# Optimization experiments

Hardware: AMD Instinct MI355X
Metric: run time of the kernel (lower is better)

## Reference

```python
import jax, jax.numpy as jnp
import numpy as np

N, E, G, T, H, ED, IN_D, OUT_D = 50000, 1600000, 64, 5, 64, 9, 10, 3
EPS = 1e-6

def _seg_mean(vals, seg, num):
    s = jax.ops.segment_sum(vals, seg, num_segments=num)
    c = jax.ops.segment_sum(jnp.ones((vals.shape[0],), vals.dtype), seg, num_segments=num)
    return s / jnp.maximum(c, 1.0)[:, None], c

def per_graph_edge_norm(edge_attr, edge_graph, num_graphs):
    # standardize each edge-feature column per graph (zero-shot transfer trick)
    mu, _ = _seg_mean(edge_attr, edge_graph, num_graphs)
    sq, _ = _seg_mean(edge_attr * edge_attr, edge_graph, num_graphs)
    var = jnp.maximum(sq - mu * mu, 0.0)
    std = jnp.sqrt(var)
    return (edge_attr - mu[edge_graph]) / (std[edge_graph] + EPS)

def setup_inputs() -> dict:
    key = jax.random.key(0)
    ks = jax.random.split(key, 24)
    s = 0.05  # weight scale to keep ReLU chains stable
    inp = {
        'x': jax.random.normal(ks[0], (N, IN_D), jnp.float32),
        'edge_index': jax.random.randint(ks[1], (2, E), 0, N),
        'edge_attr': jax.random.normal(ks[2], (E, ED), jnp.float32),
        'batch': jnp.sort(jax.random.randint(ks[3], (N,), 0, G)),
        'lift_W1': jax.random.normal(ks[4], (IN_D, H), jnp.float32) * s,
        'lift_b1': jnp.zeros((H,), jnp.float32),
        'lift_W2': jax.random.normal(ks[5], (H, H), jnp.float32) * s,
        'lift_b2': jnp.zeros((H,), jnp.float32),
        'Wself': jax.random.normal(ks[6], (T, H, H), jnp.float32) * s,
        'bself': jnp.zeros((T, H), jnp.float32),
        'msg_W0': jax.random.normal(ks[7], (T, H + ED, H), jnp.float32) * s,
        'msg_b0': jnp.zeros((T, H), jnp.float32),
        'msg_W1': jax.random.normal(ks[8], (T, H, H), jnp.float32) * s,
        'msg_b1': jnp.zeros((T, H), jnp.float32),
        'msg_W2': jax.random.normal(ks[9], (T, H, H), jnp.float32) * s,
        'msg_b2': jnp.zeros((T, H), jnp.float32),
        'gate_W': jax.random.normal(ks[10], (T, 1, H), jnp.float32) * s,
        'gate_b': jnp.zeros((T, H), jnp.float32),
        'proj_W1': jax.random.normal(ks[11], (H, H), jnp.float32) * s,
        'proj_b1': jnp.zeros((H,), jnp.float32),
        'proj_W2': jax.random.normal(ks[12], (H, OUT_D), jnp.float32) * s,
        'proj_b2': jnp.zeros((OUT_D,), jnp.float32),
    }
    return inp

def _gno(x, edge_index, edge_attr, batch,
         lift_W1, lift_b1, lift_W2, lift_b2,
         Wself, bself, msg_W0, msg_b0, msg_W1, msg_b1, msg_W2, msg_b2,
         gate_W, gate_b, proj_W1, proj_b1, proj_W2, proj_b2):
    src, dst = edge_index[0], edge_index[1]
    edge_graph = batch[src]
    ea = per_graph_edge_norm(edge_attr, edge_graph, G)  # cols 0:9 == all cols
    log_diag_y = x[:, 4:5]                               # [N,1]
    v0 = jax.nn.relu(x @ lift_W1 + lift_b1) @ lift_W2 + lift_b2  # lift
    v = v0
    for t in range(T):
        # gather -> per-edge MLP -> scatter-mean (AdmittanceKernelLayer)
        h = jnp.concatenate([v[src], ea], axis=-1)              # [E, H+ED]
        h = jax.nn.relu(h @ msg_W0[t] + msg_b0[t])
        h = jax.nn.relu(h @ msg_W1[t] + msg_b1[t])
        m = h @ msg_W2[t] + msg_b2[t]                           # [E, H]
        agg, _ = _seg_mean(m, dst, N)                           # mean aggregation
        gate = jax.nn.sigmoid(log_diag_y @ gate_W[t] + gate_b[t])  # [N,H]
        v = jax.nn.relu(v @ Wself[t] + bself[t] + agg + v0) * gate
        # dropout inactive at inference
    out = jax.nn.relu(v @ proj_W1 + proj_b1) @ proj_W2 + proj_b2  # project
    return out

def reference(x, edge_index, edge_attr, batch,
              lift_W1, lift_b1, lift_W2, lift_b2,
              Wself, bself, msg_W0, msg_b0, msg_W1, msg_b1, msg_W2, msg_b2,
              gate_W, gate_b, proj_W1, proj_b1, proj_W2, proj_b2):
    return _gno(x, edge_index, edge_attr, batch,
                lift_W1, lift_b1, lift_W2, lift_b2,
                Wself, bself, msg_W0, msg_b0, msg_W1, msg_b1, msg_W2, msg_b2,
                gate_W, gate_b, proj_W1, proj_b1, proj_W2, proj_b2)
```

## Files before the change

### kernel.cpp

```cpp
#include <hip/hip_runtime.h>
#include <math.h>

#define NN 50000
#define NE 1600000
#define NG 64
#define NT 5
#define NH 64
#define NED 9
#define NIN 10
#define NOUT 3
#define EPSF 1e-6f
#define NSUB (NE / 16)

typedef __attribute__((ext_vector_type(8))) short s8v;
typedef __attribute__((ext_vector_type(4))) short s4v;
typedef __attribute__((ext_vector_type(4))) float f32x4;

__device__ __forceinline__ unsigned short f2bf(float f) {
    union { float f; unsigned int u; } v; v.f = f;
    unsigned int r = v.u + 0x7FFFu + ((v.u >> 16) & 1u);
    return (unsigned short)(r >> 16);
}
__device__ __forceinline__ float bf2f(unsigned short b) {
    union { unsigned int u; float f; } v; v.u = ((unsigned int)b) << 16;
    return v.f;
}

__global__ void stats_kernel(const int* __restrict__ ei, const float* __restrict__ ea,
                             const int* __restrict__ batch,
                             float* __restrict__ ssum, float* __restrict__ ssq,
                             float* __restrict__ scnt, int* __restrict__ ecnt) {
    __shared__ float lsum[NG * NED];
    __shared__ float lsq[NG * NED];
    __shared__ float lcnt[NG];
    for (int i = threadIdx.x; i < NG * NED; i += blockDim.x) { lsum[i] = 0.f; lsq[i] = 0.f; }
    for (int i = threadIdx.x; i < NG; i += blockDim.x) lcnt[i] = 0.f;
    __syncthreads();
    int lane = threadIdx.x & 63;
    int stride = gridDim.x * blockDim.x;
    for (int e = blockIdx.x * blockDim.x + threadIdx.x; e < NE; e += stride) {
        int s = ei[e];
        int g = batch[s];
        atomicAdd(&ecnt[ei[NE + e]], 1);
        float a[NED];
#pragma unroll
        for (int d = 0; d < NED; ++d) a[d] = ea[(size_t)e * NED + d];
        int g0 = __builtin_amdgcn_readfirstlane(g);
        if (__all(g == g0)) {
            float sv[NED], qv[NED];
#pragma unroll
            for (int d = 0; d < NED; ++d) { sv[d] = a[d]; qv[d] = a[d] * a[d]; }
#pragma unroll
            for (int off = 32; off; off >>= 1) {
#pragma unroll
                for (int d = 0; d < NED; ++d) {
                    sv[d] += __shfl_down(sv[d], off);
                    qv[d] += __shfl_down(qv[d], off);
                }
            }
            if (lane == 0) {
#pragma unroll
                for (int d = 0; d < NED; ++d) {
                    atomicAdd(&lsum[g0 * NED + d], sv[d]);
                    atomicAdd(&lsq[g0 * NED + d], qv[d]);
                }
                atomicAdd(&lcnt[g0], 64.f);
            }
        } else {
            atomicAdd(&lcnt[g], 1.0f);
#pragma unroll
            for (int d = 0; d < NED; ++d) {
                atomicAdd(&lsum[g * NED + d], a[d]);
                atomicAdd(&lsq[g * NED + d], a[d] * a[d]);
            }
        }
    }
    __syncthreads();
    for (int i = threadIdx.x; i < NG * NED; i += blockDim.x) {
        atomicAdd(&ssum[i], lsum[i]);
        atomicAdd(&ssq[i], lsq[i]);
    }
    for (int i = threadIdx.x; i < NG; i += blockDim.x) atomicAdd(&scnt[i], lcnt[i]);
}

__global__ void stats_fin(const float* __restrict__ ssum, const float* __restrict__ ssq,
                          const float* __restrict__ scnt,
                          float* __restrict__ mu, float* __restrict__ rstd) {
    int i = blockIdx.x * blockDim.x + threadIdx.x;
    if (i >= NG * NED) return;
    int g = i / NED;
    float c = fmaxf(scnt[g], 1.0f);
    float m = ssum[i] / c;
    float q = ssq[i] / c;
    float var = fmaxf(q - m * m, 0.f);
    mu[i] = m;
    rstd[i] = 1.0f / (sqrtf(var) + EPSF);
}

__global__ void scan1_kernel(const int* __restrict__ ecnt, int* __restrict__ partial) {
    __shared__ int sm[256];
    int i = blockIdx.x * 256 + threadIdx.x;
    sm[threadIdx.x] = (i < NN) ? ecnt[i] : 0;
    __syncthreads();
    for (int off = 128; off; off >>= 1) {
        if (threadIdx.x < off) sm[threadIdx.x] += sm[threadIdx.x + off];
        __syncthreads();
    }
    if (threadIdx.x == 0) partial[blockIdx.x] = sm[0];
}
__global__ void scan2_kernel(int* __restrict__ partial, int nb) {
    __shared__ int sm[256];
    int t = threadIdx.x;
    sm[t] = (t < nb) ? partial[t] : 0;
    __syncthreads();
    for (int off = 1; off < 256; off <<= 1) {
        int v = (t >= off) ? sm[t - off] : 0;
        __syncthreads();
        sm[t] += v;
        __syncthreads();
    }
    if (t < nb) partial[t] = (t ? sm[t - 1] : 0);
}
__global__ void scan3_kernel(const int* __restrict__ ecnt, const int* __restrict__ partial,
                             int* __restrict__ offs) {
    __shared__ int sm[256];
    int b = blockIdx.x, t = threadIdx.x, i = b * 256 + t;
    int x = (i < NN) ? ecnt[i] : 0;
    sm[t] = x;
    __syncthreads();
    for (int off = 1; off < 256; off <<= 1) {
        int v = (t >= off) ? sm[t - off] : 0;
        __syncthreads();
        sm[t] += v;
        __syncthreads();
    }
    if (i < NN) offs[i] = sm[t] - x + partial[b];
}

__global__ void permute_kernel(const int* __restrict__ ei, const int* __restrict__ offs,
                               int* __restrict__ cursor, int* __restrict__ perm) {
    int stride = gridDim.x * blockDim.x;
    for (int e = blockIdx.x * blockDim.x + threadIdx.x; e < NE; e += stride) {
        int d = ei[NE + e];
        int pos = offs[d] + atomicAdd(&cursor[d], 1);
        perm[pos] = e;
    }
}

__global__ void pack_kernel(const int* __restrict__ perm, const int* __restrict__ ei,
                            const float* __restrict__ ea, const int* __restrict__ batch,
                            const float* __restrict__ mu, const float* __restrict__ rstd,
                            int* __restrict__ srcPerm, int* __restrict__ dstPerm,
                            unsigned short* __restrict__ eaN) {
    int stride = gridDim.x * blockDim.x;
    for (int p = blockIdx.x * blockDim.x + threadIdx.x; p < NE; p += stride) {
        int e = perm[p];
        int s = ei[e], d = ei[NE + e];
        int g = batch[s];
        srcPerm[p] = s;
        dstPerm[p] = d;
#pragma unroll
        for (int k = 0; k < NED; ++k) {
            float val = (ea[(size_t)e * NED + k] - mu[g * NED + k]) * rstd[g * NED + k];
            eaN[(size_t)k * NE + p] = f2bf(val);
        }
    }
}

__global__ __launch_bounds__(256) void lift_kernel(
    const float* __restrict__ x,
    const float* __restrict__ W1, const float* __restrict__ b1,
    const float* __restrict__ W2, const float* __restrict__ b2,
    float* __restrict__ v0, float* __restrict__ v, float* __restrict__ ldy) {
    __shared__ float sW1[NIN * NH];
    __shared__ __align__(16) float sW2[NH][NH];
    __shared__ float sb1[NH], sb2[NH];
    for (int i = threadIdx.x; i < NIN * NH; i += blockDim.x) sW1[i] = W1[i];
    for (int i = threadIdx.x; i < NH * NH; i += blockDim.x) {
        int k = i >> 6, j = i & 63;
        sW2[j][k] = W2[i];
    }
    for (int i = threadIdx.x; i < NH; i += blockDim.x) { sb1[i] = b1[i]; sb2[i] = b2[i]; }
    __syncthreads();
    int stride = gridDim.x * blockDim.x;
    for (int n = blockIdx.x * blockDim.x + threadIdx.x; n < NN; n += stride) {
        float xr[NIN];
#pragma unroll
        for (int k = 0; k < NIN; ++k) xr[k] = x[(size_t)n * NIN + k];
        ldy[n] = xr[4];
        float h[NH];
#pragma unroll
        for (int j = 0; j < NH; ++j) {
            float acc = sb1[j];
#pragma unroll
            for (int k = 0; k < NIN; ++k) acc += xr[k] * sW1[k * NH + j];
            h[j] = fmaxf(acc, 0.f);
        }
#pragma unroll
        for (int j = 0; j < NH; ++j) {
            float acc = sb2[j];
#pragma unroll
            for (int k = 0; k < NH; k += 4) {
                float4 w = *(const float4*)&sW2[j][k];
                acc += h[k] * w.x + h[k + 1] * w.y + h[k + 2] * w.z + h[k + 3] * w.w;
            }
            v0[(size_t)n * NH + j] = acc;
            v[(size_t)n * NH + j] = acc;
        }
    }
}

__device__ __forceinline__ void gemm_acc68(const float* __restrict__ Ab,
                                           const float* __restrict__ Wb,
                                           int K, int te, int tj, float acc[4][4]) {
#pragma unroll 4
    for (int k = 0; k < K; ++k) {
        float4 a = *(const float4*)(Ab + k * 68 + (te << 2));
        float4 b = *(const float4*)(Wb + (k << 6) + (tj << 2));
        acc[0][0] = fmaf(a.x, b.x, acc[0][0]);
        acc[0][1] = fmaf(a.x, b.y, acc[0][1]);
        acc[0][2] = fmaf(a.x, b.z, acc[0][2]);
        acc[0][3] = fmaf(a.x, b.w, acc[0][3]);
        acc[1][0] = fmaf(a.y, b.x, acc[1][0]);
        acc[1][1] = fmaf(a.y, b.y, acc[1][1]);
        acc[1][2] = fmaf(a.y, b.z, acc[1][2]);
        acc[1][3] = fmaf(a.y, b.w, acc[1][3]);
        acc[2][0] = fmaf(a.z, b.x, acc[2][0]);
        acc[2][1] = fmaf(a.z, b.y, acc[2][1]);
        acc[2][2] = fmaf(a.z, b.z, acc[2][2]);
        acc[2][3] = fmaf(a.z, b.w, acc[2][3]);
        acc[3][0] = fmaf(a.w, b.x, acc[3][0]);
        acc[3][1] = fmaf(a.w, b.y, acc[3][1]);
        acc[3][2] = fmaf(a.w, b.z, acc[3][2]);
        acc[3][3] = fmaf(a.w, b.w, acc[3][3]);
    }
}

__global__ __launch_bounds__(256, 4) void u_kernel(
    const float* __restrict__ v, const float* __restrict__ W0v,
    const float* __restrict__ b0, float* __restrict__ U) {
    __shared__ __align__(16) float Vt[64][68];
    __shared__ __align__(16) float sW[64][64];
    __shared__ float sb[64];
    const int tid = threadIdx.x;
    const int base = blockIdx.x * 64;
    const int te = tid >> 4, tj = tid & 15;

    {
        int r = tid >> 2;
        int kb = (tid & 3) << 4;
        int n = base + r;
        const float4* vrow = (const float4*)(v + (size_t)n * NH + kb);
#pragma unroll
        for (int q = 0; q < 4; ++q) {
            float4 f = (n < NN) ? vrow[q] : make_float4(0.f, 0.f, 0.f, 0.f);
            int k = kb + q * 4;
            Vt[k + 0][r] = f.x; Vt[k + 1][r] = f.y; Vt[k + 2][r] = f.z; Vt[k + 3][r] = f.w;
        }
    }
    for (int i4 = tid; i4 < 64 * 16; i4 += 256) {
        int k = i4 >> 4, c4 = i4 & 15;
        *(float4*)&sW[k][c4 * 4] = *(const float4*)(W0v + (size_t)k * 64 + c4 * 4);
    }
    if (tid < 64) sb[tid] = b0[tid];
    __syncthreads();

    float acc[4][4];
    {
        float b0_ = sb[tj * 4 + 0], b1_ = sb[tj * 4 + 1], b2_ = sb[tj * 4 + 2], b3_ = sb[tj * 4 + 3];
#pragma unroll
        for (int ee = 0; ee < 4; ++ee) { acc[ee][0] = b0_; acc[ee][1] = b1_; acc[ee][2] = b2_; acc[ee][3] = b3_; }
    }
    gemm_acc68(&Vt[0][0], &sW[0][0], 64, te, tj, acc);

#pragma unroll
    for (int ee = 0; ee < 4; ++ee) {
        int n = base + te * 4 + ee;
        if (n < NN)
            *(float4*)&U[(size_t)n * NH + tj * 4] =
                make_float4(acc[ee][0], acc[ee][1], acc[ee][2], acc[ee][3]);
    }
}

__global__ __launch_bounds__(256, 4) void edge4_kernel(
    const int* __restrict__ srcPerm, const int* __restrict__ dstPerm,
    const unsigned short* __restrict__ eaN,
    const float* __restrict__ W0e, const float* __restrict__ W1, const float* __restrict__ b1,
    const float* __restrict__ U, float* __restrict__ nodesum) {
    __shared__ __align__(16) float sWe[NED][64];
    __shared__ __align__(16) short W1frag[8][64][8];
    __shared__ __align__(16) short h0bf[4][16 * 64];
    __shared__ __align__(16) float h1s[4][16 * 64];
    __shared__ int sDstS[4][16];

    const int tid = threadIdx.x;
    const int lane = tid & 63, w = tid >> 6;
    const int l15 = lane & 15, l4 = lane >> 4;

    for (int i4 = tid; i4 < NED * 16; i4 += 256) {
        int k = i4 >> 4, c4 = i4 & 15;
        *(float4*)&sWe[k][c4 * 4] = *(const float4*)(W0e + (size_t)k * 64 + c4 * 4);
    }
    for (int idx = tid; idx < 2 * 4 * 64; idx += 256) {
        int kc = idx >> 8, c = (idx >> 6) & 3, ln = idx & 63;
        int fl15 = ln & 15, fl4 = ln >> 4;
        int col = 16 * c + fl15;
        s8v frag;
#pragma unroll
        for (int j = 0; j < 8; ++j) {
            int k = kc * 32 + fl4 * 8 + j;
            frag[j] = (short)f2bf(W1[(size_t)k * 64 + col]);
        }
        *(s8v*)&W1frag[kc * 4 + c][ln][0] = frag;
    }
    float b1r[4];
#pragma unroll
    for (int c = 0; c < 4; ++c) b1r[c] = b1[16 * c + l15];
    __syncthreads();

    short* myh0 = h0bf[w];
    float* myh1 = h1s[w];
    int*   myd  = sDstS[w];
    const int gw = blockIdx.x * 4 + w;
    const int nw = gridDim.x * 4;

    for (int st = gw; st < NSUB; st += nw) {
        const int e16 = st * 16;
        if (lane < 16) myd[lane] = dstPerm[e16 + lane];

        int4 s4 = *(const int4*)(srcPerm + e16 + 4 * l4);
        ushort4 eu[NED];
#pragma unroll
        for (int d = 0; d < NED; ++d)
            eu[d] = *(const ushort4*)(eaN + (size_t)d * NE + e16 + 4 * l4);

        float acc0[4][4];
        {
            const int* sp = (const int*)&s4;
#pragma unroll
            for (int ee = 0; ee < 4; ++ee) {
                float4 u4 = *(const float4*)(U + (size_t)sp[ee] * NH + 4 * l15);
                acc0[ee][0] = u4.x; acc0[ee][1] = u4.y; acc0[ee][2] = u4.z; acc0[ee][3] = u4.w;
            }
        }
#pragma unroll
        for (int d = 0; d < NED; ++d) {
            float4 wv = *(const float4*)&sWe[d][4 * l15];
            float a0 = bf2f(eu[d].x), a1 = bf2f(eu[d].y), a2 = bf2f(eu[d].z), a3 = bf2f(eu[d].w);
            acc0[0][0] = fmaf(a0, wv.x, acc0[0][0]); acc0[0][1] = fmaf(a0, wv.y, acc0[0][1]);
            acc0[0][2] = fmaf(a0, wv.z, acc0[0][2]); acc0[0][3] = fmaf(a0, wv.w, acc0[0][3]);
            acc0[1][0] = fmaf(a1, wv.x, acc0[1][0]); acc0[1][1] = fmaf(a1, wv.y, acc0[1][1]);
            acc0[1][2] = fmaf(a1, wv.z, acc0[1][2]); acc0[1][3] = fmaf(a1, wv.w, acc0[1][3]);
            acc0[2][0] = fmaf(a2, wv.x, acc0[2][0]); acc0[2][1] = fmaf(a2, wv.y, acc0[2][1]);
            acc0[2][2] = fmaf(a2, wv.z, acc0[2][2]); acc0[2][3] = fmaf(a2, wv.w, acc0[2][3]);
            acc0[3][0] = fmaf(a3, wv.x, acc0[3][0]); acc0[3][1] = fmaf(a3, wv.y, acc0[3][1]);
            acc0[3][2] = fmaf(a3, wv.z, acc0[3][2]); acc0[3][3] = fmaf(a3, wv.w, acc0[3][3]);
        }

#pragma unroll
        for (int ee = 0; ee < 4; ++ee) {
            int row = 4 * l4 + ee;
            s4v p;
            p[0] = (short)f2bf(fmaxf(acc0[ee][0], 0.f));
            p[1] = (short)f2bf(fmaxf(acc0[ee][1], 0.f));
            p[2] = (short)f2bf(fmaxf(acc0[ee][2], 0.f));
            p[3] = (short)f2bf(fmaxf(acc0[ee][3], 0.f));
            *(s4v*)((char*)myh0 + row * 128 + ((l15 * 8) ^ ((row & 7) << 4))) = p;
        }

        f32x4 acc[4];
#pragma unroll
        for (int c = 0; c < 4; ++c) {
            float b = b1r[c];
            acc[c][0] = b; acc[c][1] = b; acc[c][2] = b; acc[c][3] = b;
        }
        {
            const char* abase = (const char*)myh0 + l15 * 128;
            const int aswz = (l15 & 7) << 4;
#pragma unroll
            for (int kc = 0; kc < 2; ++kc) {
                s8v af = *(const s8v*)(abase + ((l4 * 16 + kc * 64) ^ aswz));
#pragma unroll
                for (int c = 0; c < 4; ++c) {
                    s8v bf = *(const s8v*)&W1frag[kc * 4 + c][lane][0];
                    acc[c] = __builtin_amdgcn_mfma_f32_16x16x32_bf16(af, bf, acc[c], 0, 0, 0);
                }
            }
        }

        int dFirst = myd[0];
        int dLast = myd[15];
        if (dFirst == dLast) {
#pragma unroll
            for (int c = 0; c < 4; ++c) {
                float vs = fmaxf(acc[c][0], 0.f) + fmaxf(acc[c][1], 0.f) +
                           fmaxf(acc[c][2], 0.f) + fmaxf(acc[c][3], 0.f);
                vs += __shfl_xor(vs, 16);
                vs += __shfl_xor(vs, 32);
                if (l4 == 0)
                    atomicAdd(&nodesum[(size_t)dFirst * NH + 16 * c + l15], vs);
            }
        } else {
#pragma unroll
            for (int r = 0; r < 4; ++r) {
                int row = 4 * l4 + r;
#pragma unroll
                for (int c = 0; c < 4; ++c)
                    myh1[row * 64 + ((16 * c + l15) ^ (l4 * 8))] = fmaxf(acc[c][r], 0.f);
            }
            int cur = dFirst;
            float a = myh1[lane];
#pragma unroll
            for (int i = 1; i < 16; ++i) {
                int dn = myd[i];
                float hv = myh1[i * 64 + (lane ^ ((i >> 2) * 8))];
                if (dn != cur) {
                    atomicAdd(&nodesum[(size_t)cur * NH + lane], a);
                    cur = dn;
                    a = hv;
                } else {
                    a += hv;
                }
            }
            atomicAdd(&nodesum[(size_t)cur * NH + lane], a);
        }
    }
}

__global__ __launch_bounds__(256, 2) void update3_kernel(
    const float* __restrict__ Wself, const float* __restrict__ bself,
    const float* __restrict__ W2, const float* __restrict__ b2,
    const float* __restrict__ gWt, const float* __restrict__ gbt,
    const float* __restrict__ v0, const float* __restrict__ ldy,
    const int* __restrict__ ecnt, const float* __restrict__ nodesum,
    float* __restrict__ v) {
    __shared__ __align__(16) float Vt[64][68];
    __shared__ __align__(16) float St[64][68];
    __shared__ __align__(16) float sWs[64][64];
    __shared__ __align__(16) float sW2[64][64];
    __shared__ float sbs[64], sb2[64], sgw[64], sgb[64];
    const int tid = threadIdx.x;
    const int base = blockIdx.x * 64;
    const int te = tid >> 4, tj = tid & 15;

    {
        int r = tid >> 2;
        int kb = (tid & 3) << 4;
        int n = base + r;
        const float4* vrow = (const float4*)(v + (size_t)n * NH + kb);
        const float4* srow = (const float4*)(nodesum + (size_t)n * NH + kb);
#pragma unroll
        for (int q = 0; q < 4; ++q) {
            float4 f = (n < NN) ? vrow[q] : make_float4(0.f, 0.f, 0.f, 0.f);
            float4 g = (n < NN) ? srow[q] : make_float4(0.f, 0.f, 0.f, 0.f);
            int k = kb + q * 4;
            Vt[k + 0][r] = f.x; Vt[k + 1][r] = f.y; Vt[k + 2][r] = f.z; Vt[k + 3][r] = f.w;
            St[k + 0][r] = g.x; St[k + 1][r] = g.y; St[k + 2][r] = g.z; St[k + 3][r] = g.w;
        }
    }
    for (int i4 = tid; i4 < 64 * 16; i4 += 256) {
        int k = i4 >> 4, c4 = i4 & 15;
        *(float4*)&sWs[k][c4 * 4] = *(const float4*)(Wself + (size_t)k * 64 + c4 * 4);
        *(float4*)&sW2[k][c4 * 4] = *(const float4*)(W2 + (size_t)k * 64 + c4 * 4);
    }
    if (tid < 64) { sbs[tid] = bself[tid]; sb2[tid] = b2[tid]; sgw[tid] = gWt[tid]; sgb[tid] = gbt[tid]; }
    __syncthreads();

    float acc1[4][4], acc2[4][4];
    {
        float b0_ = sbs[tj * 4 + 0], b1_ = sbs[tj * 4 + 1], b2_ = sbs[tj * 4 + 2], b3_ = sbs[tj * 4 + 3];
#pragma unroll
        for (int ee = 0; ee < 4; ++ee) {
            acc1[ee][0] = b0_; acc1[ee][1] = b1_; acc1[ee][2] = b2_; acc1[ee][3] = b3_;
            acc2[ee][0] = 0.f; acc2[ee][1] = 0.f; acc2[ee][2] = 0.f; acc2[ee][3] = 0.f;
        }
    }
    gemm_acc68(&Vt[0][0], &sWs[0][0], 64, te, tj, acc1);
    gemm_acc68(&St[0][0], &sW2[0][0], 64, te, tj, acc2);

    float gw0 = sgw[tj * 4 + 0], gw1 = sgw[tj * 4 + 1], gw2 = sgw[tj * 4 + 2], gw3 = sgw[tj * 4 + 3];
    float gb0 = sgb[tj * 4 + 0], gb1 = sgb[tj * 4 + 1], gb2 = sgb[tj * 4 + 2], gb3 = sgb[tj * 4 + 3];
    float bb0 = sb2[tj * 4 + 0], bb1 = sb2[tj * 4 + 1], bb2 = sb2[tj * 4 + 2], bb3 = sb2[tj * 4 + 3];
#pragma unroll
    for (int ee = 0; ee < 4; ++ee) {
        int n = base + te * 4 + ee;
        if (n >= NN) continue;
        float cnt = (float)ecnt[n];
        float has = (cnt > 0.5f) ? 1.f : 0.f;
        float dninv = has / fmaxf(cnt, 1.f);
        float ld = ldy[n];
        float4 v0r = *(const float4*)&v0[(size_t)n * NH + tj * 4];
        float z0 = acc1[ee][0] + acc2[ee][0] * dninv + bb0 * has + v0r.x;
        float z1 = acc1[ee][1] + acc2[ee][1] * dninv + bb1 * has + v0r.y;
        float z2 = acc1[ee][2] + acc2[ee][2] * dninv + bb2 * has + v0r.z;
        float z3 = acc1[ee][3] + acc2[ee][3] * dninv + bb3 * has + v0r.w;
        float g0 = 1.f / (1.f + expf(-(ld * gw0 + gb0)));
        float g1 = 1.f / (1.f + expf(-(ld * gw1 + gb1)));
        float g2 = 1.f / (1.f + expf(-(ld * gw2 + gb2)));
        float g3 = 1.f / (1.f + expf(-(ld * gw3 + gb3)));
        *(float4*)&v[(size_t)n * NH + tj * 4] =
            make_float4(fmaxf(z0, 0.f) * g0, fmaxf(z1, 0.f) * g1,
                        fmaxf(z2, 0.f) * g2, fmaxf(z3, 0.f) * g3);
    }
}

__global__ __launch_bounds__(256) void proj_kernel(
    const float* __restrict__ v,
    const float* __restrict__ pW1, const float* __restrict__ pb1,
    const float* __restrict__ pW2, const float* __restrict__ pb2,
    float* __restrict__ out) {
    __shared__ __align__(16) float sW1[NH][NH];
    __shared__ float sb1[NH];
    __shared__ float sW2[NH * NOUT];
    __shared__ float sb2[NOUT];
    for (int i = threadIdx.x; i < NH * NH; i += blockDim.x) {
        int k = i >> 6, j = i & 63;
        sW1[j][k] = pW1[i];
    }
    for (int i = threadIdx.x; i < NH; i += blockDim.x) sb1[i] = pb1[i];
    for (int i = threadIdx.x; i < NH * NOUT; i += blockDim.x) sW2[i] = pW2[i];
    for (int i = threadIdx.x; i < NOUT; i += blockDim.x) sb2[i] = pb2[i];
    __syncthreads();
    int stride = gridDim.x * blockDim.x;
    for (int n = blockIdx.x * blockDim.x + threadIdx.x; n < NN; n += stride) {
        float vr[NH];
        const float4* vp = (const float4*)(v + (size_t)n * NH);
#pragma unroll
        for (int q = 0; q < NH / 4; ++q) {
            float4 f = vp[q];
            vr[4 * q + 0] = f.x; vr[4 * q + 1] = f.y; vr[4 * q + 2] = f.z; vr[4 * q + 3] = f.w;
        }
        float o0 = sb2[0], o1 = sb2[1], o2 = sb2[2];
#pragma unroll
        for (int j = 0; j < NH; ++j) {
            float acc = sb1[j];
#pragma unroll
            for (int k = 0; k < NH; k += 4) {
                float4 w = *(const float4*)&sW1[j][k];
                acc += vr[k] * w.x + vr[k + 1] * w.y + vr[k + 2] * w.z + vr[k + 3] * w.w;
            }
            float h = fmaxf(acc, 0.f);
            o0 += h * sW2[j * NOUT + 0];
            o1 += h * sW2[j * NOUT + 1];
            o2 += h * sW2[j * NOUT + 2];
        }
        out[(size_t)n * NOUT + 0] = o0;
        out[(size_t)n * NOUT + 1] = o1;
        out[(size_t)n * NOUT + 2] = o2;
    }
}

extern "C" void kernel_launch(void* const* d_in, const int* in_sizes, int n_in,
                              void* d_out, int out_size, void* d_ws, size_t ws_size,
                              hipStream_t stream) {
    (void)in_sizes; (void)n_in; (void)out_size; (void)ws_size;
    const float* x     = (const float*)d_in[0];
    const int*   ei    = (const int*)d_in[1];
    const float* ea    = (const float*)d_in[2];
    const int*   batch = (const int*)d_in[3];
    const float* lW1   = (const float*)d_in[4];
    const float* lb1   = (const float*)d_in[5];
    const float* lW2   = (const float*)d_in[6];
    const float* lb2   = (const float*)d_in[7];
    const float* Wself = (const float*)d_in[8];
    const float* bself = (const float*)d_in[9];
    const float* mW0   = (const float*)d_in[10];
    const float* mb0   = (const float*)d_in[11];
    const float* mW1   = (const float*)d_in[12];
    const float* mb1   = (const float*)d_in[13];
    const float* mW2   = (const float*)d_in[14];
    const float* mb2   = (const float*)d_in[15];
    const float* gW    = (const float*)d_in[16];
    const float* gb    = (const float*)d_in[17];
    const float* pW1   = (const float*)d_in[18];
    const float* pb1   = (const float*)d_in[19];
    const float* pW2   = (const float*)d_in[20];
    const float* pb2   = (const float*)d_in[21];
    float* out = (float*)d_out;
    float* ws  = (float*)d_ws;

    float* nodesum = ws;
    float* v0   = nodesum + (size_t)NN * NH;
    float* v    = v0 + (size_t)NN * NH;
    float* U    = v + (size_t)NN * NH;
    float* ldy  = U + (size_t)NN * NH;
    float* mu   = ldy + NN;
    float* rstd = mu + NG * NED;
    float* ssum = rstd + NG * NED;
    float* ssq  = ssum + NG * NED;
    float* scnt = ssq + NG * NED;
    int*   ecnt   = (int*)(scnt + NG);
    int*   cursor = ecnt + NN;
    int*   offs    = cursor + NN;
    int*   partial = offs + NN;
    int*   srcPerm = partial + 256;
    int*   dstPerm = srcPerm + NE;
    unsigned short* eaN = (unsigned short*)(dstPerm + NE);
    int*   perm = (int*)nodesum;

    const int NBLK = (NN + 63) / 64;
    const int SBLK = (NN + 255) / 256;

    hipMemsetAsync(ssum, 0, ((size_t)(2 * NG * NED + NG) + 2 * NN) * sizeof(float), stream);

    stats_kernel<<<512, 256, 0, stream>>>(ei, ea, batch, ssum, ssq, scnt, ecnt);
    stats_fin<<<3, 256, 0, stream>>>(ssum, ssq, scnt, mu, rstd);
    scan1_kernel<<<SBLK, 256, 0, stream>>>(ecnt, partial);
    scan2_kernel<<<1, 256, 0, stream>>>(partial, SBLK);
    scan3_kernel<<<SBLK, 256, 0, stream>>>(ecnt, partial, offs);
    permute_kernel<<<2048, 256, 0, stream>>>(ei, offs, cursor, perm);
    pack_kernel<<<2048, 256, 0, stream>>>(perm, ei, ea, batch, mu, rstd, srcPerm, dstPerm, eaN);
    lift_kernel<<<200, 256, 0, stream>>>(x, lW1, lb1, lW2, lb2, v0, v, ldy);

    for (int t = 0; t < NT; ++t) {
        const float* W0t = mW0 + (size_t)t * (NH + NED) * NH;
        hipMemsetAsync(nodesum, 0, (size_t)NN * NH * sizeof(float), stream);
        u_kernel<<<NBLK, 256, 0, stream>>>(v, W0t, mb0 + (size_t)t * NH, U);
        edge4_kernel<<<1024, 256, 0, stream>>>(
            srcPerm, dstPerm, eaN,
            W0t + (size_t)NH * NH,
            mW1 + (size_t)t * NH * NH, mb1 + (size_t)t * NH,
            U, nodesum);
        update3_kernel<<<NBLK, 256, 0, stream>>>(
            Wself + (size_t)t * NH * NH, bself + (size_t)t * NH,
            mW2 + (size_t)t * NH * NH, mb2 + (size_t)t * NH,
            gW + (size_t)t * NH, gb + (size_t)t * NH,
            v0, ldy, ecnt, nodesum, v);
    }
    proj_kernel<<<200, 256, 0, stream>>>(v, pW1, pb1, pW2, pb2, out);
}
```

Baseline: 1.366 ms.

## Store U in bf16, prefetch next edge tile, and deterministic per-block stats reduction

The per-node U projection is now written as bf16, halving the bytes the edge kernel gathers per source node. The edge kernel software-prefetches the next tile's source indices, destinations and edge features into registers, and keeps destinations in a register read via shuffles instead of LDS. The stats kernel drops the wave-uniform shuffle reduction, writes per-block partials without global atomics, and adds a merge kernel that sums them. Trade-offs are bf16 rounding of U, extra register pressure from prefetching, and a serial merge loop over 1024 blocks.

```diff
diff --git a/kernel.cpp b/kernel.cpp
--- a/kernel.cpp
+++ b/kernel.cpp
@@ -11,6 +11,8 @@
 #define NOUT 3
 #define EPSF 1e-6f
 #define NSUB (NE / 16)
+#define STATS_BLKS 1024
+#define STATS_SLICE (2 * NG * NED + NG)
 
 typedef __attribute__((ext_vector_type(8))) short s8v;
 typedef __attribute__((ext_vector_type(4))) short s4v;
@@ -26,61 +28,48 @@
     return v.f;
 }
 
-__global__ void stats_kernel(const int* __restrict__ ei, const float* __restrict__ ea,
-                             const int* __restrict__ batch,
-                             float* __restrict__ ssum, float* __restrict__ ssq,
-                             float* __restrict__ scnt, int* __restrict__ ecnt) {
+__global__ __launch_bounds__(256) void stats_kernel(
+    const int* __restrict__ ei, const float* __restrict__ ea,
+    const int* __restrict__ batch,
+    float* __restrict__ blockAcc, int* __restrict__ ecnt) {
     __shared__ float lsum[NG * NED];
     __shared__ float lsq[NG * NED];
     __shared__ float lcnt[NG];
     for (int i = threadIdx.x; i < NG * NED; i += blockDim.x) { lsum[i] = 0.f; lsq[i] = 0.f; }
     for (int i = threadIdx.x; i < NG; i += blockDim.x) lcnt[i] = 0.f;
     __syncthreads();
-    int lane = threadIdx.x & 63;
     int stride = gridDim.x * blockDim.x;
     for (int e = blockIdx.x * blockDim.x + threadIdx.x; e < NE; e += stride) {
         int s = ei[e];
         int g = batch[s];
         atomicAdd(&ecnt[ei[NE + e]], 1);
-        float a[NED];
-#pragma unroll
-        for (int d = 0; d < NED; ++d) a[d] = ea[(size_t)e * NED + d];
-        int g0 = __builtin_amdgcn_readfirstlane(g);
-        if (__all(g == g0)) {
-            float sv[NED], qv[NED];
-#pragma unroll
-            for (int d = 0; d < NED; ++d) { sv[d] = a[d]; qv[d] = a[d] * a[d]; }
-#pragma unroll
-            for (int off = 32; off; off >>= 1) {
-#pragma unroll
-                for (int d = 0; d < NED; ++d) {
-                    sv[d] += __shfl_down(sv[d], off);
-                    qv[d] += __shfl_down(qv[d], off);
-                }
-            }
-            if (lane == 0) {
-#pragma unroll
-                for (int d = 0; d < NED; ++d) {
-                    atomicAdd(&lsum[g0 * NED + d], sv[d]);
-                    atomicAdd(&lsq[g0 * NED + d], qv[d]);
-                }
-                atomicAdd(&lcnt[g0], 64.f);
-            }
-        } else {
-            atomicAdd(&lcnt[g], 1.0f);
-#pragma unroll
-            for (int d = 0; d < NED; ++d) {
-                atomicAdd(&lsum[g * NED + d], a[d]);
-                atomicAdd(&lsq[g * NED + d], a[d] * a[d]);
-            }
-        }
-    }
-    __syncthreads();
+        atomicAdd(&lcnt[g], 1.0f);
+#pragma unroll
+        for (int d = 0; d < NED; ++d) {
+            float a = ea[(size_t)e * NED + d];
+            atomicAdd(&lsum[g * NED + d], a);
+            atomicAdd(&lsq[g * NED + d], a * a);
+        }
+    }
+    __syncthreads();
+    float* dst = blockAcc + (size_t)blockIdx.x * STATS_SLICE;
     for (int i = threadIdx.x; i < NG * NED; i += blockDim.x) {
-        atomicAdd(&ssum[i], lsum[i]);
-        atomicAdd(&ssq[i], lsq[i]);
-    }
-    for (int i = threadIdx.x; i < NG; i += blockDim.x) atomicAdd(&scnt[i], lcnt[i]);
+        dst[i] = lsum[i];
+        dst[NG * NED + i] = lsq[i];
+    }
+    for (int i = threadIdx.x; i < NG; i += blockDim.x) dst[2 * NG * NED + i] = lcnt[i];
+}
+
+__global__ void stats_merge(const float* __restrict__ blockAcc,
+                            float* __restrict__ ssum, float* __restrict__ ssq,
+                            float* __restrict__ scnt) {
+    int i = blockIdx.x * 256 + threadIdx.x;
+    if (i >= STATS_SLICE) return;
+    float a = 0.f;
+    for (int b = 0; b < STATS_BLKS; ++b) a += blockAcc[(size_t)b * STATS_SLICE + i];
+    if (i < NG * NED) ssum[i] = a;
+    else if (i < 2 * NG * NED) ssq[i - NG * NED] = a;
+    else scnt[i - 2 * NG * NED] = a;
 }
 
 __global__ void stats_fin(const float* __restrict__ ssum, const float* __restrict__ ssq,
@@ -238,7 +227,7 @@
 
 __global__ __launch_bounds__(256, 4) void u_kernel(
     const float* __restrict__ v, const float* __restrict__ W0v,
-    const float* __restrict__ b0, float* __restrict__ U) {
+    const float* __restrict__ b0, unsigned short* __restrict__ Ubf) {
     __shared__ __align__(16) float Vt[64][68];
     __shared__ __align__(16) float sW[64][64];
     __shared__ float sb[64];
@@ -276,22 +265,26 @@
 #pragma unroll
     for (int ee = 0; ee < 4; ++ee) {
         int n = base + te * 4 + ee;
-        if (n < NN)
-            *(float4*)&U[(size_t)n * NH + tj * 4] =
-                make_float4(acc[ee][0], acc[ee][1], acc[ee][2], acc[ee][3]);
-    }
-}
-
-__global__ __launch_bounds__(256, 4) void edge4_kernel(
+        if (n < NN) {
+            s4v p;
+            p[0] = (short)f2bf(acc[ee][0]);
+            p[1] = (short)f2bf(acc[ee][1]);
+            p[2] = (short)f2bf(acc[ee][2]);
+            p[3] = (short)f2bf(acc[ee][3]);
+            *(s4v*)&Ubf[(size_t)n * NH + tj * 4] = p;
+        }
+    }
+}
+
+__global__ __launch_bounds__(256, 4) void edge5_kernel(
     const int* __restrict__ srcPerm, const int* __restrict__ dstPerm,
     const unsigned short* __restrict__ eaN,
     const float* __restrict__ W0e, const float* __restrict__ W1, const float* __restrict__ b1,
-    const float* __restrict__ U, float* __restrict__ nodesum) {
+    const unsigned short* __restrict__ Ubf, float* __restrict__ nodesum) {
     __shared__ __align__(16) float sWe[NED][64];
     __shared__ __align__(16) short W1frag[8][64][8];
     __shared__ __align__(16) short h0bf[4][16 * 64];
     __shared__ __align__(16) float h1s[4][16 * 64];
-    __shared__ int sDstS[4][16];
 
     const int tid = threadIdx.x;
     const int lane = tid & 63, w = tid >> 6;
@@ -320,33 +313,45 @@
 
     short* myh0 = h0bf[w];
     float* myh1 = h1s[w];
-    int*   myd  = sDstS[w];
     const int gw = blockIdx.x * 4 + w;
     const int nw = gridDim.x * 4;
+    if (gw >= NSUB) return;
+
+    int e16 = gw * 16;
+    int4 s4 = *(const int4*)(srcPerm + e16 + 4 * l4);
+    int dreg = dstPerm[e16 + l15];
+    ushort4 eu[NED];
+#pragma unroll
+    for (int d = 0; d < NED; ++d)
+        eu[d] = *(const ushort4*)(eaN + (size_t)d * NE + e16 + 4 * l4);
 
     for (int st = gw; st < NSUB; st += nw) {
-        const int e16 = st * 16;
-        if (lane < 16) myd[lane] = dstPerm[e16 + lane];
-
-        int4 s4 = *(const int4*)(srcPerm + e16 + 4 * l4);
-        ushort4 eu[NED];
-#pragma unroll
-        for (int d = 0; d < NED; ++d)
-            eu[d] = *(const ushort4*)(eaN + (size_t)d * NE + e16 + 4 * l4);
-
-        float acc0[4][4];
+        s4v uv[4];
         {
             const int* sp = (const int*)&s4;
 #pragma unroll
-            for (int ee = 0; ee < 4; ++ee) {
-                float4 u4 = *(const float4*)(U + (size_t)sp[ee] * NH + 4 * l15);
-                acc0[ee][0] = u4.x; acc0[ee][1] = u4.y; acc0[ee][2] = u4.z; acc0[ee][3] = u4.w;
-            }
+            for (int ee = 0; ee < 4; ++ee)
+                uv[ee] = *(const s4v*)(Ubf + (size_t)sp[ee] * NH + 4 * l15);
+        }
+        int stn = st + nw;
+        int e16n = ((stn < NSUB) ? stn : st) * 16;
+        int4 s4n = *(const int4*)(srcPerm + e16n + 4 * l4);
+        int dregn = dstPerm[e16n + l15];
+        ushort4 eun[NED];
+#pragma unroll
+        for (int d = 0; d < NED; ++d)
+            eun[d] = *(const ushort4*)(eaN + (size_t)d * NE + e16n + 4 * l4);
+
+        float acc0[4][4];
+#pragma unroll
+        for (int ee = 0; ee < 4; ++ee) {
+            acc0[ee][0] = 0.f; acc0[ee][1] = 0.f; acc0[ee][2] = 0.f; acc0[ee][3] = 0.f;
         }
 #pragma unroll
         for (int d = 0; d < NED; ++d) {
             float4 wv = *(const float4*)&sWe[d][4 * l15];
-            float a0 = bf2f(eu[d].x), a1 = bf2f(eu[d].y), a2 = bf2f(eu[d].z), a3 = bf2f(eu[d].w);
+            float a0 = bf2f((unsigned short)eu[d].x), a1 = bf2f((unsigned short)eu[d].y);
+            float a2 = bf2f((unsigned short)eu[d].z), a3 = bf2f((unsigned short)eu[d].w);
             acc0[0][0] = fmaf(a0, wv.x, acc0[0][0]); acc0[0][1] = fmaf(a0, wv.y, acc0[0][1]);
             acc0[0][2] = fmaf(a0, wv.z, acc0[0][2]); acc0[0][3] = fmaf(a0, wv.w, acc0[0][3]);
             acc0[1][0] = fmaf(a1, wv.x, acc0[1][0]); acc0[1][1] = fmaf(a1, wv.y, acc0[1][1]);
@@ -356,6 +361,13 @@
             acc0[3][0] = fmaf(a3, wv.x, acc0[3][0]); acc0[3][1] = fmaf(a3, wv.y, acc0[3][1]);
             acc0[3][2] = fmaf(a3, wv.z, acc0[3][2]); acc0[3][3] = fmaf(a3, wv.w, acc0[3][3]);
         }
+#pragma unroll
+        for (int ee = 0; ee < 4; ++ee) {
+            acc0[ee][0] += bf2f((unsigned short)uv[ee][0]);
+            acc0[ee][1] += bf2f((unsigned short)uv[ee][1]);
+            acc0[ee][2] += bf2f((unsigned short)uv[ee][2]);
+            acc0[ee][3] += bf2f((unsigned short)uv[ee][3]);
+        }
 
 #pragma unroll
         for (int ee = 0; ee < 4; ++ee) {
@@ -388,8 +400,8 @@
             }
         }
 
-        int dFirst = myd[0];
-        int dLast = myd[15];
+        int dFirst = __shfl(dreg, 0);
+        int dLast = __shfl(dreg, 15);
         if (dFirst == dLast) {
 #pragma unroll
             for (int c = 0; c < 4; ++c) {
@@ -412,7 +424,7 @@
             float a = myh1[lane];
 #pragma unroll
             for (int i = 1; i < 16; ++i) {
-                int dn = myd[i];
+                int dn = __shfl(dreg, i);
                 float hv = myh1[i * 64 + (lane ^ ((i >> 2) * 8))];
                 if (dn != cur) {
                     atomicAdd(&nodesum[(size_t)cur * NH + lane], a);
@@ -424,6 +436,11 @@
             }
             atomicAdd(&nodesum[(size_t)cur * NH + lane], a);
         }
+
+        s4 = s4n;
+        dreg = dregn;
+#pragma unroll
+        for (int d = 0; d < NED; ++d) eu[d] = eun[d];
     }
 }
 
@@ -582,8 +599,8 @@
     float* nodesum = ws;
     float* v0   = nodesum + (size_t)NN * NH;
     float* v    = v0 + (size_t)NN * NH;
-    float* U    = v + (size_t)NN * NH;
-    float* ldy  = U + (size_t)NN * NH;
+    unsigned short* Ubf = (unsigned short*)(v + (size_t)NN * NH);
+    float* ldy  = (float*)Ubf + (size_t)NN * NH;
     float* mu   = ldy + NN;
     float* rstd = mu + NG * NED;
     float* ssum = rstd + NG * NED;
@@ -596,14 +613,16 @@
     int*   srcPerm = partial + 256;
     int*   dstPerm = srcPerm + NE;
     unsigned short* eaN = (unsigned short*)(dstPerm + NE);
+    float* statsPart = (float*)(eaN + (size_t)NED * NE);
     int*   perm = (int*)nodesum;
 
     const int NBLK = (NN + 63) / 64;
     const int SBLK = (NN + 255) / 256;
 
-    hipMemsetAsync(ssum, 0, ((size_t)(2 * NG * NED + NG) + 2 * NN) * sizeof(float), stream);
-
-    stats_kernel<<<512, 256, 0, stream>>>(ei, ea, batch, ssum, ssq, scnt, ecnt);
+    hipMemsetAsync(ecnt, 0, (size_t)2 * NN * sizeof(int), stream);
+
+    stats_kernel<<<STATS_BLKS, 256, 0, stream>>>(ei, ea, batch, statsPart, ecnt);
+    stats_merge<<<(STATS_SLICE + 255) / 256, 256, 0, stream>>>(statsPart, ssum, ssq, scnt);
     stats_fin<<<3, 256, 0, stream>>>(ssum, ssq, scnt, mu, rstd);
     scan1_kernel<<<SBLK, 256, 0, stream>>>(ecnt, partial);
     scan2_kernel<<<1, 256, 0, stream>>>(partial, SBLK);
@@ -615,12 +634,12 @@
     for (int t = 0; t < NT; ++t) {
         const float* W0t = mW0 + (size_t)t * (NH + NED) * NH;
         hipMemsetAsync(nodesum, 0, (size_t)NN * NH * sizeof(float), stream);
-        u_kernel<<<NBLK, 256, 0, stream>>>(v, W0t, mb0 + (size_t)t * NH, U);
-        edge4_kernel<<<1024, 256, 0, stream>>>(
+        u_kernel<<<NBLK, 256, 0, stream>>>(v, W0t, mb0 + (size_t)t * NH, Ubf);
+        edge5_kernel<<<1024, 256, 0, stream>>>(
             srcPerm, dstPerm, eaN,
             W0t + (size_t)NH * NH,
             mW1 + (size_t)t * NH * NH, mb1 + (size_t)t * NH,
-            U, nodesum);
+            Ubf, nodesum);
         update3_kernel<<<NBLK, 256, 0, stream>>>(
             Wself + (size_t)t * NH * NH, bself + (size_t)t * NH,
             mW2 + (size_t)t * NH * NH, mb2 + (size_t)t * NH,
```

New measurement: 1.649 ms. 20.7% more time.
